# Performance work log

Hardware: AMD Instinct MI355X
Metric: run time of the kernel (lower is better)

Reference implementation:

```python
import jax, jax.numpy as jnp
import numpy as np
from jax import lax

NUM_HEADS = 4
DIM = 192
EPS = 1e-12  # torch F.normalize eps


def setup_inputs() -> dict:
    key = jax.random.key(0)
    ks = jax.random.split(key, 5)
    b, c, h, w = 8, DIM, 128, 128
    x = jax.random.normal(ks[0], (b, c, h, w), dtype=jnp.float32)
    f = jax.random.normal(ks[1], (b, c, h, w), dtype=jnp.float32)
    # conv weights, scaled like kaiming-ish init
    w_qkv = jax.random.normal(ks[2], (3 * c, c, 1, 1), dtype=jnp.float32) * (1.0 / np.sqrt(c))
    w_dw = jax.random.normal(ks[3], (3 * c, 1, 3, 3), dtype=jnp.float32) * (1.0 / 3.0)
    w_proj = jax.random.normal(ks[4], (c, c, 1, 1), dtype=jnp.float32) * (1.0 / np.sqrt(c))
    temperature = jnp.ones((NUM_HEADS, 1, 1), dtype=jnp.float32)
    return {"x": x, "f": f, "w_qkv": w_qkv, "w_dw": w_dw, "w_proj": w_proj,
            "temperature": temperature}


def _conv(x, w, groups=1):
    return lax.conv_general_dilated(
        x, w, window_strides=(1, 1), padding="SAME",
        dimension_numbers=("NCHW", "OIHW", "NCHW"),
        feature_group_count=groups)


def reference(x, f, w_qkv, w_dw, w_proj, temperature):
    b, c, h, w = x.shape
    x_in = x + f
    qkv = _conv(x_in, w_qkv)                 # [b, 3c, h, w] 1x1 conv
    qkv = _conv(qkv, w_dw, groups=3 * c)     # depthwise 3x3
    q, k, v = jnp.split(qkv, 3, axis=1)      # each [b, c, h, w]
    hw = h * w
    ch = c // NUM_HEADS

    def heads(t):
        return t.reshape(b, NUM_HEADS, ch, hw)  # 'b (head c) h w -> b head c (h w)'

    q, k, v = heads(q), heads(k), heads(v)
    # L2-normalize over spatial (last) dim, torch-style eps clamp
    q = q / jnp.maximum(jnp.linalg.norm(q, axis=-1, keepdims=True), EPS)
    k = k / jnp.maximum(jnp.linalg.norm(k, axis=-1, keepdims=True), EPS)
    # transposed (channel) attention: [b, head, ch, ch]
    attn = jnp.einsum("bhcn,bhdn->bhcd", q, k) * temperature[None]
    attn = jax.nn.softmax(attn, axis=-1)
    out = jnp.einsum("bhcd,bhdn->bhcn", attn, v)  # [b, head, ch, hw]
    out = out.reshape(b, c, h, w)
    return _conv(out, w_proj)
```

## Files before the change

### kernel.cpp

```cpp
#include <hip/hip_runtime.h>
#include <stdint.h>

#define NB 8
#define NC 192
#define NOC 576
#define NH 4
#define HW 16384
#define NCHUNK 16

typedef unsigned short u16;
typedef __bf16 v8bf __attribute__((ext_vector_type(8)));
typedef float v4f __attribute__((ext_vector_type(4)));
typedef u16 v8us __attribute__((ext_vector_type(8)));
typedef u16 v4us __attribute__((ext_vector_type(4)));

__device__ __forceinline__ u16 f2bf(float f) {
    uint32_t u = __float_as_uint(f);
    u += 0x7FFFu + ((u >> 16) & 1u);
    return (u16)(u >> 16);
}
__device__ __forceinline__ float bf2f(u16 u) {
    return __uint_as_float(((uint32_t)u) << 16);
}

__global__ void k_cvt_w(const float* __restrict__ w, u16* __restrict__ wb, int n) {
    int i = blockIdx.x * 256 + threadIdx.x;
    if (i < n) wb[i] = f2bf(w[i]);
}

__global__ __launch_bounds__(256, 2) void k_gemm_qkv(
    const float* __restrict__ x, const float* __restrict__ f,
    const u16* __restrict__ wb, u16* __restrict__ qkv, int b0)
{
    __shared__ u16 bt[64 * 192];
    __shared__ u16 wt[576 * 32];
    const int t = threadIdx.x;
    const int bl = blockIdx.y;
    const int bg = b0 + bl;
    const int p0 = blockIdx.x * 64;

    {
        const int px = t & 63;
        const int cg = t >> 6;
        #pragma unroll
        for (int it = 0; it < 6; ++it) {
            const int c4 = it * 4 + cg;
            const size_t base = ((size_t)bg * NC + c4 * 8) * HW + p0 + px;
            v8us pk;
            #pragma unroll
            for (int j = 0; j < 8; ++j) {
                float v = x[base + (size_t)j * HW] + f[base + (size_t)j * HW];
                pk[j] = f2bf(v);
            }
            *reinterpret_cast<v8us*>(&bt[px * 192 + ((c4 ^ (px & 7)) << 3)]) = pk;
        }
    }

    const int w = t >> 6, l = t & 63, lr = l & 15, lg = l >> 4;
    const int oc0 = w * 144;

    v4f acc[4][9];
    #pragma unroll
    for (int mi = 0; mi < 4; ++mi)
        #pragma unroll
        for (int ni = 0; ni < 9; ++ni)
            acc[mi][ni] = (v4f){0.f, 0.f, 0.f, 0.f};

    #pragma unroll 1
    for (int ks = 0; ks < 6; ++ks) {
        __syncthreads();
        #pragma unroll
        for (int it = 0; it < 9; ++it) {
            const int idx = it * 256 + t;
            const int oc = idx >> 2, lgw = idx & 3;
            v8us wv = *reinterpret_cast<const v8us*>(&wb[oc * 192 + ks * 32 + lgw * 8]);
            *reinterpret_cast<v8us*>(&wt[oc * 32 + ((lgw ^ ((oc >> 1) & 3)) << 3)]) = wv;
        }
        __syncthreads();

        v8bf a[4];
        #pragma unroll
        for (int mi = 0; mi < 4; ++mi) {
            const int px = mi * 16 + lr;
            a[mi] = *reinterpret_cast<const v8bf*>(&bt[px * 192 + (((ks * 4 + lg) ^ (px & 7)) << 3)]);
        }
        #pragma unroll
        for (int ni = 0; ni < 9; ++ni) {
            const int oc = oc0 + ni * 16 + lr;
            const v8bf bw = *reinterpret_cast<const v8bf*>(&wt[oc * 32 + ((lg ^ ((oc >> 1) & 3)) << 3)]);
            #pragma unroll
            for (int mi = 0; mi < 4; ++mi)
                acc[mi][ni] = __builtin_amdgcn_mfma_f32_16x16x32_bf16(a[mi], bw, acc[mi][ni], 0, 0, 0);
        }
    }

    #pragma unroll
    for (int mi = 0; mi < 4; ++mi)
        #pragma unroll
        for (int ni = 0; ni < 9; ++ni) {
            const int oc = oc0 + ni * 16 + lr;
            const int px = p0 + mi * 16 + lg * 4;
            v4us pk;
            pk[0] = f2bf(acc[mi][ni][0]); pk[1] = f2bf(acc[mi][ni][1]);
            pk[2] = f2bf(acc[mi][ni][2]); pk[3] = f2bf(acc[mi][ni][3]);
            *reinterpret_cast<v4us*>(&qkv[((size_t)bl * NOC + oc) * HW + px]) = pk;
        }
}

__global__ __launch_bounds__(256) void k_dw(
    const u16* __restrict__ qkv, const float* __restrict__ wdw,
    u16* __restrict__ qk_out, u16* __restrict__ v_out,
    float* __restrict__ sumsq, int b0)
{
    __shared__ u16 plane[128 * 136];
    __shared__ float red[4];
    const int t = threadIdx.x;
    const int ch = blockIdx.x;
    const int bl = blockIdx.y;
    const int bg = b0 + bl;
    const size_t pbase = ((size_t)bl * NOC + ch) * HW;

    float wk[9];
    #pragma unroll
    for (int i = 0; i < 9; ++i) wk[i] = wdw[ch * 9 + i];

    const int r = t >> 1;
    const int cb = (t & 1) * 64;

    #pragma unroll
    for (int i = 0; i < 8; ++i) {
        v8us v = *reinterpret_cast<const v8us*>(&qkv[pbase + r * 128 + cb + i * 8]);
        *reinterpret_cast<v8us*>(&plane[r * 136 + cb + i * 8]) = v;
    }
    __syncthreads();

    const bool vm = (r > 0), vp = (r < 127);
    const u16* rowm = &plane[(r - 1) * 136];
    const u16* rowc = &plane[r * 136];
    const u16* rowp = &plane[(r + 1) * 136];

    float am, ac, bm, bc, cm, cc2;
    if (cb == 0) { am = 0.f; bm = 0.f; cm = 0.f; }
    else {
        am = vm ? bf2f(rowm[cb - 1]) : 0.f;
        bm = bf2f(rowc[cb - 1]);
        cm = vp ? bf2f(rowp[cb - 1]) : 0.f;
    }
    ac = vm ? bf2f(rowm[cb]) : 0.f;
    bc = bf2f(rowc[cb]);
    cc2 = vp ? bf2f(rowp[cb]) : 0.f;

    uint32_t ov[32];
    float ssq = 0.f;
    #pragma unroll
    for (int xp = 0; xp < 32; ++xp) {
        #pragma unroll
        for (int s2 = 0; s2 < 2; ++s2) {
            const int col = cb + xp * 2 + s2;
            float ap, bp, cp;
            if (col < 127) {
                ap = vm ? bf2f(rowm[col + 1]) : 0.f;
                bp = bf2f(rowc[col + 1]);
                cp = vp ? bf2f(rowp[col + 1]) : 0.f;
            } else { ap = 0.f; bp = 0.f; cp = 0.f; }
            float o = wk[0]*am + wk[1]*ac + wk[2]*ap
                    + wk[3]*bm + wk[4]*bc + wk[5]*bp
                    + wk[6]*cm + wk[7]*cc2 + wk[8]*cp;
            u16 ob = f2bf(o);
            float orr = bf2f(ob);
            ssq += orr * orr;
            ov[xp] = (s2 == 0) ? (uint32_t)ob : (ov[xp] | ((uint32_t)ob << 16));
            am = ac; ac = ap; bm = bc; bc = bp; cm = cc2; cc2 = cp;
        }
    }

    __syncthreads();
    #pragma unroll
    for (int i = 0; i < 32; ++i)
        *reinterpret_cast<uint32_t*>(&plane[r * 136 + cb + i * 2]) = ov[i];
    __syncthreads();

    u16* dst = (ch < 2 * NC) ? (qk_out + ((size_t)bg * (2 * NC) + ch) * HW)
                             : (v_out + ((size_t)bg * NC + (ch - 2 * NC)) * HW);
    #pragma unroll
    for (int i = 0; i < 8; ++i) {
        const int idx = i * 2048 + t * 8;
        const int rr = idx >> 7, cc = idx & 127;
        v8us v = *reinterpret_cast<const v8us*>(&plane[rr * 136 + cc]);
        *reinterpret_cast<v8us*>(&dst[idx]) = v;
    }

    #pragma unroll
    for (int off = 32; off > 0; off >>= 1) ssq += __shfl_down(ssq, off);
    if ((t & 63) == 0) red[t >> 6] = ssq;
    __syncthreads();
    if (t == 0 && ch < 2 * NC) sumsq[bg * (2 * NC) + ch] = red[0] + red[1] + red[2] + red[3];
}

__global__ __launch_bounds__(256) void k_attn(
    const u16* __restrict__ qk, float* __restrict__ partials)
{
    __shared__ float wsum[4 * 2304];
    const int t = threadIdx.x;
    const int chunk = blockIdx.x;
    const int h = blockIdx.y;
    const int b = blockIdx.z;
    const int w = t >> 6, l = t & 63, lr = l & 15, lg = l >> 4;

    const size_t qbase = ((size_t)b * 384 + h * 48) * HW;
    const size_t kbase = ((size_t)b * 384 + 192 + h * 48) * HW;
    const int pb = chunk * 1024 + w * 256;

    v4f acc[3][3];
    #pragma unroll
    for (int mi = 0; mi < 3; ++mi)
        #pragma unroll
        for (int ni = 0; ni < 3; ++ni)
            acc[mi][ni] = (v4f){0.f, 0.f, 0.f, 0.f};

    #pragma unroll
    for (int ks = 0; ks < 8; ++ks) {
        const int k = pb + ks * 32 + lg * 8;
        v8bf a[3], bb[3];
        #pragma unroll
        for (int mi = 0; mi < 3; ++mi)
            a[mi] = *reinterpret_cast<const v8bf*>(&qk[qbase + (size_t)(mi * 16 + lr) * HW + k]);
        #pragma unroll
        for (int ni = 0; ni < 3; ++ni)
            bb[ni] = *reinterpret_cast<const v8bf*>(&qk[kbase + (size_t)(ni * 16 + lr) * HW + k]);
        #pragma unroll
        for (int mi = 0; mi < 3; ++mi)
            #pragma unroll
            for (int ni = 0; ni < 3; ++ni)
                acc[mi][ni] = __builtin_amdgcn_mfma_f32_16x16x32_bf16(a[mi], bb[ni], acc[mi][ni], 0, 0, 0);
    }

    #pragma unroll
    for (int mi = 0; mi < 3; ++mi)
        #pragma unroll
        for (int ni = 0; ni < 3; ++ni)
            #pragma unroll
            for (int r = 0; r < 4; ++r)
                wsum[w * 2304 + (mi * 16 + lg * 4 + r) * 48 + ni * 16 + lr] = acc[mi][ni][r];
    __syncthreads();

    #pragma unroll
    for (int i = 0; i < 9; ++i) {
        const int e = t + i * 256;
        float s = wsum[e] + wsum[2304 + e] + wsum[4608 + e] + wsum[6912 + e];
        partials[(((size_t)(b * NH + h)) * NCHUNK + chunk) * 2304 + e] = s;
    }
}

__global__ __launch_bounds__(256) void k_smx(
    const float* __restrict__ partials, const float* __restrict__ sumsq,
    const float* __restrict__ wproj, const float* __restrict__ temp,
    u16* __restrict__ Mb)
{
    __shared__ float att[2304];
    __shared__ float rq[48], rk[48];
    const int t = threadIdx.x;
    const int h = blockIdx.x;
    const int b = blockIdx.y;

    if (t < 48) {
        float s = sumsq[b * 384 + h * 48 + t];
        rq[t] = 1.f / fmaxf(sqrtf(s), 1e-12f);
    } else if (t < 96) {
        float s = sumsq[b * 384 + 192 + h * 48 + (t - 48)];
        rk[t - 48] = 1.f / fmaxf(sqrtf(s), 1e-12f);
    }
    __syncthreads();
    const float tp = temp[h];
    #pragma unroll
    for (int i = 0; i < 9; ++i) {
        const int e = t + i * 256;
        const float* pp = &partials[(((size_t)(b * NH + h)) * NCHUNK) * 2304 + e];
        float s = 0.f;
        #pragma unroll
        for (int c = 0; c < NCHUNK; ++c) s += pp[(size_t)c * 2304];
        att[e] = s * rq[e / 48] * rk[e % 48] * tp;
    }
    __syncthreads();
    if (t < 48) {
        float m = -1e30f;
        #pragma unroll
        for (int j = 0; j < 48; ++j) m = fmaxf(m, att[t * 48 + j]);
        float s = 0.f;
        for (int j = 0; j < 48; ++j) { float e2 = __expf(att[t * 48 + j] - m); att[t * 48 + j] = e2; s += e2; }
        const float inv = 1.f / s;
        for (int j = 0; j < 48; ++j) att[t * 48 + j] *= inv;
    }
    __syncthreads();
    #pragma unroll
    for (int i = 0; i < 36; ++i) {
        const int idx = t + i * 256;
        const int oc = idx / 48, d = idx % 48;
        float s = 0.f;
        #pragma unroll
        for (int cc = 0; cc < 48; ++cc)
            s += wproj[oc * 192 + h * 48 + cc] * att[cc * 48 + d];
        Mb[((size_t)b * NC + oc) * NC + h * 48 + d] = f2bf(s);
    }
}

__global__ __launch_bounds__(256) void k_gemm_out(
    const u16* __restrict__ vp, const u16* __restrict__ Mb,
    float* __restrict__ out)
{
    __shared__ u16 bt[64 * 192];
    const int t = threadIdx.x;
    const int b = blockIdx.y;
    const int p0 = blockIdx.x * 64;

    {
        const int px = t & 63;
        const int cg = t >> 6;
        #pragma unroll
        for (int it = 0; it < 6; ++it) {
            const int c4 = it * 4 + cg;
            const size_t base = ((size_t)b * NC + c4 * 8) * HW + p0 + px;
            v8us pk;
            #pragma unroll
            for (int j = 0; j < 8; ++j) pk[j] = vp[base + (size_t)j * HW];
            *reinterpret_cast<v8us*>(&bt[px * 192 + ((c4 ^ (px & 7)) << 3)]) = pk;
        }
    }
    __syncthreads();

    const int w = t >> 6, l = t & 63, lr = l & 15, lg = l >> 4;
    const int oc0 = w * 48;

    v4f acc[4][3];
    #pragma unroll
    for (int mi = 0; mi < 4; ++mi)
        #pragma unroll
        for (int ni = 0; ni < 3; ++ni)
            acc[mi][ni] = (v4f){0.f, 0.f, 0.f, 0.f};

    #pragma unroll
    for (int ks = 0; ks < 6; ++ks) {
        const int k = ks * 32 + lg * 8;
        const int c4 = ks * 4 + lg;
        v8bf a[4];
        #pragma unroll
        for (int mi = 0; mi < 4; ++mi) {
            const int px = mi * 16 + lr;
            a[mi] = *reinterpret_cast<const v8bf*>(&bt[px * 192 + ((c4 ^ (px & 7)) << 3)]);
        }
        #pragma unroll
        for (int ni = 0; ni < 3; ++ni) {
            const int oc = oc0 + ni * 16 + lr;
            const v8bf bw = *reinterpret_cast<const v8bf*>(&Mb[((size_t)b * NC + oc) * NC + k]);
            #pragma unroll
            for (int mi = 0; mi < 4; ++mi)
                acc[mi][ni] = __builtin_amdgcn_mfma_f32_16x16x32_bf16(a[mi], bw, acc[mi][ni], 0, 0, 0);
        }
    }

    #pragma unroll
    for (int mi = 0; mi < 4; ++mi)
        #pragma unroll
        for (int ni = 0; ni < 3; ++ni) {
            const int oc = oc0 + ni * 16 + lr;
            const int px = p0 + mi * 16 + lg * 4;
            *reinterpret_cast<v4f*>(&out[((size_t)b * NC + oc) * HW + px]) = acc[mi][ni];
        }
}

extern "C" void kernel_launch(void* const* d_in, const int* in_sizes, int n_in,
                              void* d_out, int out_size, void* d_ws, size_t ws_size,
                              hipStream_t stream)
{
    (void)in_sizes; (void)n_in; (void)out_size;
    const float* x      = (const float*)d_in[0];
    const float* f      = (const float*)d_in[1];
    const float* w_qkv  = (const float*)d_in[2];
    const float* w_dw   = (const float*)d_in[3];
    const float* w_proj = (const float*)d_in[4];
    const float* temp   = (const float*)d_in[5];

    char* ws = (char*)d_ws;
    u16*   vws      = (u16*)(ws);
    u16*   wb       = (u16*)(ws + 50331648);
    float* sumsq    = (float*)(ws + 50552832);
    float* partials = (float*)(ws + 50565120);
    u16*   Mb       = (u16*)(ws + 55283712);
    const size_t FIXED = 55873536;
    const size_t PERB  = (size_t)NOC * HW * 2;
    u16*   qkv_raw  = (u16*)(ws + FIXED);

    int g = 1;
    if (ws_size > FIXED + PERB) {
        size_t avail = (ws_size - FIXED) / PERB;
        g = (int)(avail > 8 ? 8 : avail);
        if (g < 1) g = 1;
    }

    u16* qk_scratch = (u16*)d_out;
    float* out      = (float*)d_out;

    hipLaunchKernelGGL(k_cvt_w, dim3(432), dim3(256), 0, stream, w_qkv, wb, NOC * NC);
    for (int b0 = 0; b0 < NB; b0 += g) {
        const int nb = (b0 + g <= NB) ? g : (NB - b0);
        hipLaunchKernelGGL(k_gemm_qkv, dim3(HW / 64, nb), dim3(256), 0, stream, x, f, wb, qkv_raw, b0);
        hipLaunchKernelGGL(k_dw, dim3(NOC, nb), dim3(256), 0, stream, qkv_raw, w_dw, qk_scratch, vws, sumsq, b0);
    }
    hipLaunchKernelGGL(k_attn, dim3(NCHUNK, NH, NB), dim3(256), 0, stream, qk_scratch, partials);
    hipLaunchKernelGGL(k_smx, dim3(NH, NB), dim3(256), 0, stream, partials, sumsq, w_proj, temp, Mb);
    hipLaunchKernelGGL(k_gemm_out, dim3(HW / 64, NB), dim3(256), 0, stream, vws, Mb, out);
}
```

Before: 333.5 us.

## Prefetch next weight slice into registers and stage qkv stores through LDS

The 1x1 conv kernel now loads the next K-slice of weights into registers while the current slice is consumed, which hides global load latency behind MFMA work. The epilogue writes accumulators into the LDS weight buffer with an XOR swizzle, then reads them back so each thread emits contiguous 16-byte global stores instead of scattered 8-byte ones. This costs 36 extra VGPRs for the prefetch buffer and two extra barrier pairs in the epilogue. The higher register pressure may lower occupancy.

```diff
diff --git a/kernel.cpp b/kernel.cpp
--- a/kernel.cpp
+++ b/kernel.cpp
@@ -66,6 +66,16 @@
         for (int ni = 0; ni < 9; ++ni)
             acc[mi][ni] = (v4f){0.f, 0.f, 0.f, 0.f};
 
+    const int widx_oc = (t * 4) >> 2;
+
+    v8us wload[9];
+    #pragma unroll
+    for (int it = 0; it < 9; ++it) {
+        const int idx = it * 256 + t;
+        const int oc = idx >> 2, lgw = idx & 3;
+        wload[it] = *reinterpret_cast<const v8us*>(&wb[oc * 192 + lgw * 8]);
+    }
+
     #pragma unroll 1
     for (int ks = 0; ks < 6; ++ks) {
         __syncthreads();
@@ -73,8 +83,15 @@
         for (int it = 0; it < 9; ++it) {
             const int idx = it * 256 + t;
             const int oc = idx >> 2, lgw = idx & 3;
-            v8us wv = *reinterpret_cast<const v8us*>(&wb[oc * 192 + ks * 32 + lgw * 8]);
-            *reinterpret_cast<v8us*>(&wt[oc * 32 + ((lgw ^ ((oc >> 1) & 3)) << 3)]) = wv;
+            *reinterpret_cast<v8us*>(&wt[oc * 32 + ((lgw ^ ((oc >> 1) & 3)) << 3)]) = wload[it];
+        }
+        if (ks < 5) {
+            #pragma unroll
+            for (int it = 0; it < 9; ++it) {
+                const int idx = it * 256 + t;
+                const int oc = idx >> 2, lgw = idx & 3;
+                wload[it] = *reinterpret_cast<const v8us*>(&wb[oc * 192 + (ks + 1) * 32 + lgw * 8]);
+            }
         }
         __syncthreads();
 
@@ -95,16 +112,39 @@
     }
 
     #pragma unroll
-    for (int mi = 0; mi < 4; ++mi)
-        #pragma unroll
-        for (int ni = 0; ni < 9; ++ni) {
-            const int oc = oc0 + ni * 16 + lr;
-            const int px = p0 + mi * 16 + lg * 4;
-            v4us pk;
-            pk[0] = f2bf(acc[mi][ni][0]); pk[1] = f2bf(acc[mi][ni][1]);
-            pk[2] = f2bf(acc[mi][ni][2]); pk[3] = f2bf(acc[mi][ni][3]);
-            *reinterpret_cast<v4us*>(&qkv[((size_t)bl * NOC + oc) * HW + px]) = pk;
-        }
+    for (int pass = 0; pass < 2; ++pass) {
+        __syncthreads();
+        #pragma unroll
+        for (int mi2 = 0; mi2 < 2; ++mi2) {
+            const int mi = pass * 2 + mi2;
+            #pragma unroll
+            for (int ni = 0; ni < 9; ++ni) {
+                const int oc = oc0 + ni * 16 + lr;
+                const int chunk = mi2 * 4 + lg;
+                const int sch = chunk ^ (oc & 3);
+                v4us pk;
+                pk[0] = f2bf(acc[mi][ni][0]); pk[1] = f2bf(acc[mi][ni][1]);
+                pk[2] = f2bf(acc[mi][ni][2]); pk[3] = f2bf(acc[mi][ni][3]);
+                *reinterpret_cast<v4us*>(&wt[oc * 32 + sch * 4]) = pk;
+            }
+        }
+        __syncthreads();
+        #pragma unroll
+        for (int rd = 0; rd < 9; ++rd) {
+            const int e = rd * 2048 + t * 8;
+            const int oc = e >> 5;
+            const int col = e & 31;
+            const int c0 = (col >> 2) ^ (oc & 3);
+            const int c1 = ((col >> 2) + 1) ^ (oc & 3);
+            v4us lo = *reinterpret_cast<v4us*>(&wt[oc * 32 + c0 * 4]);
+            v4us hi = *reinterpret_cast<v4us*>(&wt[oc * 32 + c1 * 4]);
+            v8us o8;
+            o8[0] = lo[0]; o8[1] = lo[1]; o8[2] = lo[2]; o8[3] = lo[3];
+            o8[4] = hi[0]; o8[5] = hi[1]; o8[6] = hi[2]; o8[7] = hi[3];
+            *reinterpret_cast<v8us*>(&qkv[((size_t)bl * NOC + oc) * HW + p0 + pass * 32 + col]) = o8;
+        }
+    }
+    (void)widx_oc;
 }
 
 __global__ __launch_bounds__(256) void k_dw(
```

Result: faster. 310.0 us (-7.1%).

## Use 512-thread QKV GEMM blocks with prefetched weights and LDS-staged output stores

Applied to the files above, without the earlier changes.

The QKV 1x1-conv GEMM kernel moves from 256 to 512 threads per block, splitting the 64-pixel tile across two wave groups so each wave keeps half as many accumulators. Weight K-slices are prefetched into registers one step ahead so global loads overlap the MFMA work, and the LDS swizzle for weights changes. The output is staged through shared memory so each channel row is written as contiguous 64-byte segments instead of scattered 8-byte pieces. This adds extra barriers and LDS traffic in the epilogue, and occupancy at 4 blocks per CU may be limited by the roughly 48KB of LDS each block uses.

```diff
diff --git a/kernel.cpp b/kernel.cpp
--- a/kernel.cpp
+++ b/kernel.cpp
@@ -28,7 +28,7 @@
     if (i < n) wb[i] = f2bf(w[i]);
 }
 
-__global__ __launch_bounds__(256, 2) void k_gemm_qkv(
+__global__ __launch_bounds__(512, 4) void k_gemm_qkv(
     const float* __restrict__ x, const float* __restrict__ f,
     const u16* __restrict__ wb, u16* __restrict__ qkv, int b0)
 {
@@ -43,8 +43,8 @@
         const int px = t & 63;
         const int cg = t >> 6;
         #pragma unroll
-        for (int it = 0; it < 6; ++it) {
-            const int c4 = it * 4 + cg;
+        for (int it = 0; it < 3; ++it) {
+            const int c4 = it * 8 + cg;
             const size_t base = ((size_t)bg * NC + c4 * 8) * HW + p0 + px;
             v8us pk;
             #pragma unroll
@@ -57,54 +57,96 @@
     }
 
     const int w = t >> 6, l = t & 63, lr = l & 15, lg = l >> 4;
-    const int oc0 = w * 144;
-
-    v4f acc[4][9];
-    #pragma unroll
-    for (int mi = 0; mi < 4; ++mi)
+    const int wp = w >> 2;
+    const int wo = w & 3;
+    const int oc0 = wo * 144;
+
+    v4f acc[2][9];
+    #pragma unroll
+    for (int mi = 0; mi < 2; ++mi)
         #pragma unroll
         for (int ni = 0; ni < 9; ++ni)
             acc[mi][ni] = (v4f){0.f, 0.f, 0.f, 0.f};
+
+    v8us wload[5];
+    #pragma unroll
+    for (int it = 0; it < 5; ++it) {
+        const int idx = it * 512 + t;
+        if (idx < 2304) {
+            const int oc = idx >> 2, q = idx & 3;
+            wload[it] = *reinterpret_cast<const v8us*>(&wb[oc * 192 + q * 8]);
+        }
+    }
 
     #pragma unroll 1
     for (int ks = 0; ks < 6; ++ks) {
         __syncthreads();
         #pragma unroll
-        for (int it = 0; it < 9; ++it) {
-            const int idx = it * 256 + t;
-            const int oc = idx >> 2, lgw = idx & 3;
-            v8us wv = *reinterpret_cast<const v8us*>(&wb[oc * 192 + ks * 32 + lgw * 8]);
-            *reinterpret_cast<v8us*>(&wt[oc * 32 + ((lgw ^ ((oc >> 1) & 3)) << 3)]) = wv;
+        for (int it = 0; it < 5; ++it) {
+            const int idx = it * 512 + t;
+            if (idx < 2304) {
+                const int oc = idx >> 2, q = idx & 3;
+                const int g = (oc ^ (oc >> 2)) & 3;
+                *reinterpret_cast<v8us*>(&wt[oc * 32 + ((q ^ g) << 3)]) = wload[it];
+            }
+        }
+        if (ks < 5) {
+            #pragma unroll
+            for (int it = 0; it < 5; ++it) {
+                const int idx = it * 512 + t;
+                if (idx < 2304) {
+                    const int oc = idx >> 2, q = idx & 3;
+                    wload[it] = *reinterpret_cast<const v8us*>(&wb[oc * 192 + (ks + 1) * 32 + q * 8]);
+                }
+            }
         }
         __syncthreads();
 
-        v8bf a[4];
-        #pragma unroll
-        for (int mi = 0; mi < 4; ++mi) {
-            const int px = mi * 16 + lr;
+        v8bf a[2];
+        #pragma unroll
+        for (int mi = 0; mi < 2; ++mi) {
+            const int px = wp * 32 + mi * 16 + lr;
             a[mi] = *reinterpret_cast<const v8bf*>(&bt[px * 192 + (((ks * 4 + lg) ^ (px & 7)) << 3)]);
         }
         #pragma unroll
         for (int ni = 0; ni < 9; ++ni) {
             const int oc = oc0 + ni * 16 + lr;
-            const v8bf bw = *reinterpret_cast<const v8bf*>(&wt[oc * 32 + ((lg ^ ((oc >> 1) & 3)) << 3)]);
-            #pragma unroll
-            for (int mi = 0; mi < 4; ++mi)
+            const int g = (oc ^ (oc >> 2)) & 3;
+            const v8bf bw = *reinterpret_cast<const v8bf*>(&wt[oc * 32 + ((lg ^ g) << 3)]);
+            #pragma unroll
+            for (int mi = 0; mi < 2; ++mi)
                 acc[mi][ni] = __builtin_amdgcn_mfma_f32_16x16x32_bf16(a[mi], bw, acc[mi][ni], 0, 0, 0);
         }
     }
 
     #pragma unroll
-    for (int mi = 0; mi < 4; ++mi)
-        #pragma unroll
-        for (int ni = 0; ni < 9; ++ni) {
-            const int oc = oc0 + ni * 16 + lr;
-            const int px = p0 + mi * 16 + lg * 4;
-            v4us pk;
-            pk[0] = f2bf(acc[mi][ni][0]); pk[1] = f2bf(acc[mi][ni][1]);
-            pk[2] = f2bf(acc[mi][ni][2]); pk[3] = f2bf(acc[mi][ni][3]);
-            *reinterpret_cast<v4us*>(&qkv[((size_t)bl * NOC + oc) * HW + px]) = pk;
-        }
+    for (int pass = 0; pass < 2; ++pass) {
+        __syncthreads();
+        if (wp == pass) {
+            #pragma unroll
+            for (int mi = 0; mi < 2; ++mi) {
+                #pragma unroll
+                for (int ni = 0; ni < 9; ++ni) {
+                    const int oc = oc0 + ni * 16 + lr;
+                    const int chunk = mi * 4 + lg;
+                    const int sch = chunk ^ (oc & 7);
+                    v4us pk;
+                    pk[0] = f2bf(acc[mi][ni][0]); pk[1] = f2bf(acc[mi][ni][1]);
+                    pk[2] = f2bf(acc[mi][ni][2]); pk[3] = f2bf(acc[mi][ni][3]);
+                    *reinterpret_cast<v4us*>(&wt[oc * 32 + sch * 4]) = pk;
+                }
+            }
+        }
+        __syncthreads();
+        #pragma unroll
+        for (int rd = 0; rd < 9; ++rd) {
+            const int idx = rd * 512 + t;
+            const int oc = idx >> 3;
+            const int c = idx & 7;
+            v4us v = *reinterpret_cast<v4us*>(&wt[oc * 32 + (c ^ (oc & 7)) * 4]);
+            *reinterpret_cast<v4us*>(&qkv[((size_t)bl * NOC + oc) * HW + p0 + pass * 32 + c * 4]) = v;
+        }
+    }
 }
 
 __global__ __launch_bounds__(256) void k_dw(
@@ -403,7 +445,7 @@
     hipLaunchKernelGGL(k_cvt_w, dim3(432), dim3(256), 0, stream, w_qkv, wb, NOC * NC);
     for (int b0 = 0; b0 < NB; b0 += g) {
         const int nb = (b0 + g <= NB) ? g : (NB - b0);
-        hipLaunchKernelGGL(k_gemm_qkv, dim3(HW / 64, nb), dim3(256), 0, stream, x, f, wb, qkv_raw, b0);
+        hipLaunchKernelGGL(k_gemm_qkv, dim3(HW / 64, nb), dim3(512), 0, stream, x, f, wb, qkv_raw, b0);
         hipLaunchKernelGGL(k_dw, dim3(NOC, nb), dim3(256), 0, stream, qkv_raw, w_dw, qk_scratch, vws, sumsq, b0);
     }
     hipLaunchKernelGGL(k_attn, dim3(NCHUNK, NH, NB), dim3(256), 0, stream, qk_scratch, partials);
```

Result: faster. 301.7 us (-9.5%).

## Fuse QKV 1x1 GEMM with depthwise 3x3 via row-ring shared buffer

Applied to the files above, without the earlier changes.

Replaces the separate QKV GEMM and depthwise-conv kernels with a prep kernel that writes x+f as channel-last bf16, plus a fused kernel. The fused kernel computes 1x1-conv rows into a 4-slot shared-memory ring and immediately applies the 3x3 depthwise stencil. It writes outputs in a row-group-blocked layout with per-group partial sums of squares, which the softmax kernel then reduces. This removes the round trip of the full 576-channel intermediate through global memory, at the cost of recomputing halo rows (10 rows per 8) and reading weights directly from global. The output GEMM now stages its results through LDS to make the stores coalesced.

```diff
diff --git a/kernel.cpp b/kernel.cpp
--- a/kernel.cpp
+++ b/kernel.cpp
@@ -7,6 +7,10 @@
 #define NH 4
 #define HW 16384
 #define NCHUNK 16
+#define NRG 16
+#define RPG 8
+#define NOCG 6
+#define OCG 96
 
 typedef unsigned short u16;
 typedef __bf16 v8bf __attribute__((ext_vector_type(8)));
@@ -28,173 +32,164 @@
     if (i < n) wb[i] = f2bf(w[i]);
 }
 
-__global__ __launch_bounds__(256, 2) void k_gemm_qkv(
+__global__ __launch_bounds__(256) void k_prep(
     const float* __restrict__ x, const float* __restrict__ f,
-    const u16* __restrict__ wb, u16* __restrict__ qkv, int b0)
-{
-    __shared__ u16 bt[64 * 192];
-    __shared__ u16 wt[576 * 32];
+    u16* __restrict__ xf)
+{
+    __shared__ u16 xt[128 * 200];
     const int t = threadIdx.x;
-    const int bl = blockIdx.y;
-    const int bg = b0 + bl;
-    const int p0 = blockIdx.x * 64;
-
-    {
-        const int px = t & 63;
-        const int cg = t >> 6;
-        #pragma unroll
-        for (int it = 0; it < 6; ++it) {
-            const int c4 = it * 4 + cg;
-            const size_t base = ((size_t)bg * NC + c4 * 8) * HW + p0 + px;
-            v8us pk;
-            #pragma unroll
-            for (int j = 0; j < 8; ++j) {
-                float v = x[base + (size_t)j * HW] + f[base + (size_t)j * HW];
-                pk[j] = f2bf(v);
+    const int row = blockIdx.x;
+    const int bg = blockIdx.y;
+
+    #pragma unroll
+    for (int it = 0; it < 24; ++it) {
+        const int idx = it * 256 + t;
+        const int q = idx & 31;
+        const int c = idx >> 5;
+        const size_t base = ((size_t)bg * NC + c) * HW + row * 128 + q * 4;
+        const float4 xv = *reinterpret_cast<const float4*>(&x[base]);
+        const float4 fv = *reinterpret_cast<const float4*>(&f[base]);
+        xt[(q * 4 + 0) * 200 + c] = f2bf(xv.x + fv.x);
+        xt[(q * 4 + 1) * 200 + c] = f2bf(xv.y + fv.y);
+        xt[(q * 4 + 2) * 200 + c] = f2bf(xv.z + fv.z);
+        xt[(q * 4 + 3) * 200 + c] = f2bf(xv.w + fv.w);
+    }
+    __syncthreads();
+    if (t < 192) {
+        const int co = t % 24;
+        const int pxg = t / 24;
+        #pragma unroll
+        for (int it = 0; it < 16; ++it) {
+            const int px = it * 8 + pxg;
+            v8us v = *reinterpret_cast<v8us*>(&xt[px * 200 + co * 8]);
+            *reinterpret_cast<v8us*>(&xf[((size_t)(bg * 128 + row) * 128 + px) * 192 + co * 8]) = v;
+        }
+    }
+}
+
+__global__ __launch_bounds__(512) void k_fused(
+    const u16* __restrict__ xf, const u16* __restrict__ wb,
+    const float* __restrict__ wdw,
+    u16* __restrict__ qk_t, u16* __restrict__ v_t,
+    float* __restrict__ sumsqp)
+{
+    __shared__ u16 ring[4 * 96 * 136];
+    const int t = threadIdx.x;
+    const int ocg = blockIdx.x / NRG;
+    const int rg  = blockIdx.x % NRG;
+    const int bg  = blockIdx.y;
+    const int r0 = rg * RPG;
+    const int oc_base = ocg * OCG;
+
+    const int w = t >> 6, l = t & 63, lr = l & 15, lg = l >> 4;
+    const int wpx = w & 3;
+    const int woc = w >> 1 & 0;
+    const int wo2 = w >> 2;
+
+    const int oc_l = t >> 2;
+    const int px0 = (t & 3) * 32;
+    float wk[9];
+    if (t < 384) {
+        #pragma unroll
+        for (int i = 0; i < 9; ++i) wk[i] = wdw[(oc_base + oc_l) * 9 + i];
+    }
+    float ssq = 0.f;
+
+    #pragma unroll 1
+    for (int rr = r0 - 1; rr <= r0 + RPG; ++rr) {
+        if (rr >= 0 && rr < 128) {
+            v4f acc[2][3];
+            #pragma unroll
+            for (int mi = 0; mi < 2; ++mi)
+                #pragma unroll
+                for (int ni = 0; ni < 3; ++ni)
+                    acc[mi][ni] = (v4f){0.f, 0.f, 0.f, 0.f};
+            #pragma unroll
+            for (int ks = 0; ks < 6; ++ks) {
+                v8bf a[2];
+                #pragma unroll
+                for (int mi = 0; mi < 2; ++mi)
+                    a[mi] = *reinterpret_cast<const v8bf*>(
+                        &xf[((size_t)(bg * 128 + rr) * 128 + wpx * 32 + mi * 16 + lr) * 192 + ks * 32 + lg * 8]);
+                #pragma unroll
+                for (int ni = 0; ni < 3; ++ni) {
+                    const v8bf bw = *reinterpret_cast<const v8bf*>(
+                        &wb[(size_t)(oc_base + wo2 * 48 + ni * 16 + lr) * 192 + ks * 32 + lg * 8]);
+                    #pragma unroll
+                    for (int mi = 0; mi < 2; ++mi)
+                        acc[mi][ni] = __builtin_amdgcn_mfma_f32_16x16x32_bf16(a[mi], bw, acc[mi][ni], 0, 0, 0);
+                }
             }
-            *reinterpret_cast<v8us*>(&bt[px * 192 + ((c4 ^ (px & 7)) << 3)]) = pk;
-        }
-    }
-
-    const int w = t >> 6, l = t & 63, lr = l & 15, lg = l >> 4;
-    const int oc0 = w * 144;
-
-    v4f acc[4][9];
-    #pragma unroll
-    for (int mi = 0; mi < 4; ++mi)
-        #pragma unroll
-        for (int ni = 0; ni < 9; ++ni)
-            acc[mi][ni] = (v4f){0.f, 0.f, 0.f, 0.f};
-
-    #pragma unroll 1
-    for (int ks = 0; ks < 6; ++ks) {
+            const int slot = (rr & 3) * (96 * 136);
+            #pragma unroll
+            for (int mi = 0; mi < 2; ++mi)
+                #pragma unroll
+                for (int ni = 0; ni < 3; ++ni) {
+                    const int ol = wo2 * 48 + ni * 16 + lr;
+                    const int pxw = wpx * 32 + mi * 16 + lg * 4;
+                    v4us pk;
+                    pk[0] = f2bf(acc[mi][ni][0]); pk[1] = f2bf(acc[mi][ni][1]);
+                    pk[2] = f2bf(acc[mi][ni][2]); pk[3] = f2bf(acc[mi][ni][3]);
+                    *reinterpret_cast<v4us*>(&ring[slot + ol * 136 + pxw]) = pk;
+                }
+        }
         __syncthreads();
-        #pragma unroll
-        for (int it = 0; it < 9; ++it) {
-            const int idx = it * 256 + t;
-            const int oc = idx >> 2, lgw = idx & 3;
-            v8us wv = *reinterpret_cast<const v8us*>(&wb[oc * 192 + ks * 32 + lgw * 8]);
-            *reinterpret_cast<v8us*>(&wt[oc * 32 + ((lgw ^ ((oc >> 1) & 3)) << 3)]) = wv;
-        }
-        __syncthreads();
-
-        v8bf a[4];
-        #pragma unroll
-        for (int mi = 0; mi < 4; ++mi) {
-            const int px = mi * 16 + lr;
-            a[mi] = *reinterpret_cast<const v8bf*>(&bt[px * 192 + (((ks * 4 + lg) ^ (px & 7)) << 3)]);
-        }
-        #pragma unroll
-        for (int ni = 0; ni < 9; ++ni) {
-            const int oc = oc0 + ni * 16 + lr;
-            const v8bf bw = *reinterpret_cast<const v8bf*>(&wt[oc * 32 + ((lg ^ ((oc >> 1) & 3)) << 3)]);
-            #pragma unroll
-            for (int mi = 0; mi < 4; ++mi)
-                acc[mi][ni] = __builtin_amdgcn_mfma_f32_16x16x32_bf16(a[mi], bw, acc[mi][ni], 0, 0, 0);
-        }
-    }
-
-    #pragma unroll
-    for (int mi = 0; mi < 4; ++mi)
-        #pragma unroll
-        for (int ni = 0; ni < 9; ++ni) {
-            const int oc = oc0 + ni * 16 + lr;
-            const int px = p0 + mi * 16 + lg * 4;
-            v4us pk;
-            pk[0] = f2bf(acc[mi][ni][0]); pk[1] = f2bf(acc[mi][ni][1]);
-            pk[2] = f2bf(acc[mi][ni][2]); pk[3] = f2bf(acc[mi][ni][3]);
-            *reinterpret_cast<v4us*>(&qkv[((size_t)bl * NOC + oc) * HW + px]) = pk;
-        }
-}
-
-__global__ __launch_bounds__(256) void k_dw(
-    const u16* __restrict__ qkv, const float* __restrict__ wdw,
-    u16* __restrict__ qk_out, u16* __restrict__ v_out,
-    float* __restrict__ sumsq, int b0)
-{
-    __shared__ u16 plane[128 * 136];
-    __shared__ float red[4];
-    const int t = threadIdx.x;
-    const int ch = blockIdx.x;
-    const int bl = blockIdx.y;
-    const int bg = b0 + bl;
-    const size_t pbase = ((size_t)bl * NOC + ch) * HW;
-
-    float wk[9];
-    #pragma unroll
-    for (int i = 0; i < 9; ++i) wk[i] = wdw[ch * 9 + i];
-
-    const int r = t >> 1;
-    const int cb = (t & 1) * 64;
-
-    #pragma unroll
-    for (int i = 0; i < 8; ++i) {
-        v8us v = *reinterpret_cast<const v8us*>(&qkv[pbase + r * 128 + cb + i * 8]);
-        *reinterpret_cast<v8us*>(&plane[r * 136 + cb + i * 8]) = v;
-    }
-    __syncthreads();
-
-    const bool vm = (r > 0), vp = (r < 127);
-    const u16* rowm = &plane[(r - 1) * 136];
-    const u16* rowc = &plane[r * 136];
-    const u16* rowp = &plane[(r + 1) * 136];
-
-    float am, ac, bm, bc, cm, cc2;
-    if (cb == 0) { am = 0.f; bm = 0.f; cm = 0.f; }
-    else {
-        am = vm ? bf2f(rowm[cb - 1]) : 0.f;
-        bm = bf2f(rowc[cb - 1]);
-        cm = vp ? bf2f(rowp[cb - 1]) : 0.f;
-    }
-    ac = vm ? bf2f(rowm[cb]) : 0.f;
-    bc = bf2f(rowc[cb]);
-    cc2 = vp ? bf2f(rowp[cb]) : 0.f;
-
-    uint32_t ov[32];
-    float ssq = 0.f;
-    #pragma unroll
-    for (int xp = 0; xp < 32; ++xp) {
-        #pragma unroll
-        for (int s2 = 0; s2 < 2; ++s2) {
-            const int col = cb + xp * 2 + s2;
-            float ap, bp, cp;
-            if (col < 127) {
-                ap = vm ? bf2f(rowm[col + 1]) : 0.f;
-                bp = bf2f(rowc[col + 1]);
-                cp = vp ? bf2f(rowp[col + 1]) : 0.f;
-            } else { ap = 0.f; bp = 0.f; cp = 0.f; }
-            float o = wk[0]*am + wk[1]*ac + wk[2]*ap
-                    + wk[3]*bm + wk[4]*bc + wk[5]*bp
-                    + wk[6]*cm + wk[7]*cc2 + wk[8]*cp;
-            u16 ob = f2bf(o);
-            float orr = bf2f(ob);
-            ssq += orr * orr;
-            ov[xp] = (s2 == 0) ? (uint32_t)ob : (ov[xp] | ((uint32_t)ob << 16));
-            am = ac; ac = ap; bm = bc; bc = bp; cm = cc2; cc2 = cp;
-        }
-    }
-
-    __syncthreads();
-    #pragma unroll
-    for (int i = 0; i < 32; ++i)
-        *reinterpret_cast<uint32_t*>(&plane[r * 136 + cb + i * 2]) = ov[i];
-    __syncthreads();
-
-    u16* dst = (ch < 2 * NC) ? (qk_out + ((size_t)bg * (2 * NC) + ch) * HW)
-                             : (v_out + ((size_t)bg * NC + (ch - 2 * NC)) * HW);
-    #pragma unroll
-    for (int i = 0; i < 8; ++i) {
-        const int idx = i * 2048 + t * 8;
-        const int rr = idx >> 7, cc = idx & 127;
-        v8us v = *reinterpret_cast<const v8us*>(&plane[rr * 136 + cc]);
-        *reinterpret_cast<v8us*>(&dst[idx]) = v;
-    }
-
-    #pragma unroll
-    for (int off = 32; off > 0; off >>= 1) ssq += __shfl_down(ssq, off);
-    if ((t & 63) == 0) red[t >> 6] = ssq;
-    __syncthreads();
-    if (t == 0 && ch < 2 * NC) sumsq[bg * (2 * NC) + ch] = red[0] + red[1] + red[2] + red[3];
+        const int rd = rr - 1;
+        if (rd >= r0 && rd < r0 + RPG && t < 384) {
+            const u16* rowm = &ring[((rd - 1) & 3) * (96 * 136) + oc_l * 136];
+            const u16* rowc = &ring[((rd    ) & 3) * (96 * 136) + oc_l * 136];
+            const u16* rowp = &ring[((rd + 1) & 3) * (96 * 136) + oc_l * 136];
+            const bool vm = (rd > 0), vp = (rd < 127);
+
+            float am, ac, bm, bc, cm, cc2;
+            if (px0 == 0) { am = 0.f; bm = 0.f; cm = 0.f; }
+            else {
+                am = vm ? bf2f(rowm[px0 - 1]) : 0.f;
+                bm = bf2f(rowc[px0 - 1]);
+                cm = vp ? bf2f(rowp[px0 - 1]) : 0.f;
+            }
+            ac = vm ? bf2f(rowm[px0]) : 0.f;
+            bc = bf2f(rowc[px0]);
+            cc2 = vp ? bf2f(rowp[px0]) : 0.f;
+
+            uint32_t ov[16];
+            #pragma unroll
+            for (int xp = 0; xp < 16; ++xp) {
+                #pragma unroll
+                for (int s2 = 0; s2 < 2; ++s2) {
+                    const int col = px0 + xp * 2 + s2;
+                    float ap, bp, cp;
+                    if (col < 127) {
+                        ap = vm ? bf2f(rowm[col + 1]) : 0.f;
+                        bp = bf2f(rowc[col + 1]);
+                        cp = vp ? bf2f(rowp[col + 1]) : 0.f;
+                    } else { ap = 0.f; bp = 0.f; cp = 0.f; }
+                    float o = wk[0]*am + wk[1]*ac + wk[2]*ap
+                            + wk[3]*bm + wk[4]*bc + wk[5]*bp
+                            + wk[6]*cm + wk[7]*cc2 + wk[8]*cp;
+                    u16 ob = f2bf(o);
+                    float orr = bf2f(ob);
+                    ssq += orr * orr;
+                    ov[xp] = (s2 == 0) ? (uint32_t)ob : (ov[xp] | ((uint32_t)ob << 16));
+                    am = ac; ac = ap; bm = bc; bc = bp; cm = cc2; cc2 = cp;
+                }
+            }
+
+            u16* dst = (ocg < 4)
+                ? qk_t + ((size_t)(bg * NRG + rg) * 384 + ocg * 96 + oc_l) * 1024 + (rd & 7) * 128 + px0
+                : v_t  + ((size_t)(bg * NRG + rg) * 192 + (ocg - 4) * 96 + oc_l) * 1024 + (rd & 7) * 128 + px0;
+            #pragma unroll
+            for (int k2 = 0; k2 < 4; ++k2)
+                *reinterpret_cast<uint4*>(dst + k2 * 8) = *reinterpret_cast<uint4*>(&ov[k2 * 4]);
+        }
+    }
+
+    if (ocg < 4 && t < 384) {
+        ssq += __shfl_down(ssq, 2);
+        ssq += __shfl_down(ssq, 1);
+        if ((t & 3) == 0)
+            sumsqp[((size_t)rg * NB + bg) * 384 + ocg * 96 + oc_l] = ssq;
+    }
 }
 
 __global__ __launch_bounds__(256) void k_attn(
@@ -207,9 +202,9 @@
     const int b = blockIdx.z;
     const int w = t >> 6, l = t & 63, lr = l & 15, lg = l >> 4;
 
-    const size_t qbase = ((size_t)b * 384 + h * 48) * HW;
-    const size_t kbase = ((size_t)b * 384 + 192 + h * 48) * HW;
-    const int pb = chunk * 1024 + w * 256;
+    const size_t qbase = ((size_t)(b * NRG + chunk) * 384 + h * 48) * 1024;
+    const size_t kbase = ((size_t)(b * NRG + chunk) * 384 + 192 + h * 48) * 1024;
+    const int pb = w * 256;
 
     v4f acc[3][3];
     #pragma unroll
@@ -224,10 +219,10 @@
         v8bf a[3], bb[3];
         #pragma unroll
         for (int mi = 0; mi < 3; ++mi)
-            a[mi] = *reinterpret_cast<const v8bf*>(&qk[qbase + (size_t)(mi * 16 + lr) * HW + k]);
+            a[mi] = *reinterpret_cast<const v8bf*>(&qk[qbase + (size_t)(mi * 16 + lr) * 1024 + k]);
         #pragma unroll
         for (int ni = 0; ni < 3; ++ni)
-            bb[ni] = *reinterpret_cast<const v8bf*>(&qk[kbase + (size_t)(ni * 16 + lr) * HW + k]);
+            bb[ni] = *reinterpret_cast<const v8bf*>(&qk[kbase + (size_t)(ni * 16 + lr) * 1024 + k]);
         #pragma unroll
         for (int mi = 0; mi < 3; ++mi)
             #pragma unroll
@@ -253,7 +248,7 @@
 }
 
 __global__ __launch_bounds__(256) void k_smx(
-    const float* __restrict__ partials, const float* __restrict__ sumsq,
+    const float* __restrict__ partials, const float* __restrict__ sumsqp,
     const float* __restrict__ wproj, const float* __restrict__ temp,
     u16* __restrict__ Mb)
 {
@@ -264,10 +259,16 @@
     const int b = blockIdx.y;
 
     if (t < 48) {
-        float s = sumsq[b * 384 + h * 48 + t];
+        float s = 0.f;
+        #pragma unroll
+        for (int rg = 0; rg < NRG; ++rg)
+            s += sumsqp[((size_t)rg * NB + b) * 384 + h * 48 + t];
         rq[t] = 1.f / fmaxf(sqrtf(s), 1e-12f);
     } else if (t < 96) {
-        float s = sumsq[b * 384 + 192 + h * 48 + (t - 48)];
+        float s = 0.f;
+        #pragma unroll
+        for (int rg = 0; rg < NRG; ++rg)
+            s += sumsqp[((size_t)rg * NB + b) * 384 + 192 + h * 48 + (t - 48)];
         rk[t - 48] = 1.f / fmaxf(sqrtf(s), 1e-12f);
     }
     __syncthreads();
@@ -308,10 +309,12 @@
     const u16* __restrict__ vp, const u16* __restrict__ Mb,
     float* __restrict__ out)
 {
-    __shared__ u16 bt[64 * 192];
+    __shared__ float smemf[12288];
+    u16* bt = reinterpret_cast<u16*>(smemf);
     const int t = threadIdx.x;
     const int b = blockIdx.y;
     const int p0 = blockIdx.x * 64;
+    const int row = p0 >> 7, rgo = row >> 3, rl = row & 7, c0 = p0 & 127;
 
     {
         const int px = t & 63;
@@ -319,10 +322,10 @@
         #pragma unroll
         for (int it = 0; it < 6; ++it) {
             const int c4 = it * 4 + cg;
-            const size_t base = ((size_t)b * NC + c4 * 8) * HW + p0 + px;
             v8us pk;
             #pragma unroll
-            for (int j = 0; j < 8; ++j) pk[j] = vp[base + (size_t)j * HW];
+            for (int j = 0; j < 8; ++j)
+                pk[j] = vp[((size_t)(b * NRG + rgo) * 192 + c4 * 8 + j) * 1024 + rl * 128 + c0 + px];
             *reinterpret_cast<v8us*>(&bt[px * 192 + ((c4 ^ (px & 7)) << 3)]) = pk;
         }
     }
@@ -358,21 +361,34 @@
         }
     }
 
+    __syncthreads();
+    float* et = smemf;
     #pragma unroll
     for (int mi = 0; mi < 4; ++mi)
         #pragma unroll
         for (int ni = 0; ni < 3; ++ni) {
             const int oc = oc0 + ni * 16 + lr;
-            const int px = p0 + mi * 16 + lg * 4;
-            *reinterpret_cast<v4f*>(&out[((size_t)b * NC + oc) * HW + px]) = acc[mi][ni];
-        }
+            const int u = mi * 4 + lg;
+            const int su = u ^ (oc & 15);
+            *reinterpret_cast<v4f*>(&et[oc * 64 + su * 4]) = acc[mi][ni];
+        }
+    __syncthreads();
+    #pragma unroll
+    for (int rd = 0; rd < 12; ++rd) {
+        const int idx = rd * 256 + t;
+        const int oc = idx >> 4;
+        const int u = idx & 15;
+        const int su = u ^ (oc & 15);
+        v4f v = *reinterpret_cast<v4f*>(&et[oc * 64 + su * 4]);
+        *reinterpret_cast<v4f*>(&out[((size_t)b * NC + oc) * HW + p0 + u * 4]) = v;
+    }
 }
 
 extern "C" void kernel_launch(void* const* d_in, const int* in_sizes, int n_in,
                               void* d_out, int out_size, void* d_ws, size_t ws_size,
                               hipStream_t stream)
 {
-    (void)in_sizes; (void)n_in; (void)out_size;
+    (void)in_sizes; (void)n_in; (void)out_size; (void)ws_size;
     const float* x      = (const float*)d_in[0];
     const float* f      = (const float*)d_in[1];
     const float* w_qkv  = (const float*)d_in[2];
@@ -383,30 +399,19 @@
     char* ws = (char*)d_ws;
     u16*   vws      = (u16*)(ws);
     u16*   wb       = (u16*)(ws + 50331648);
-    float* sumsq    = (float*)(ws + 50552832);
-    float* partials = (float*)(ws + 50565120);
-    u16*   Mb       = (u16*)(ws + 55283712);
-    const size_t FIXED = 55873536;
-    const size_t PERB  = (size_t)NOC * HW * 2;
-    u16*   qkv_raw  = (u16*)(ws + FIXED);
-
-    int g = 1;
-    if (ws_size > FIXED + PERB) {
-        size_t avail = (ws_size - FIXED) / PERB;
-        g = (int)(avail > 8 ? 8 : avail);
-        if (g < 1) g = 1;
-    }
-
-    u16* qk_scratch = (u16*)d_out;
-    float* out      = (float*)d_out;
+    float* sumsqp   = (float*)(ws + 50552832);
+    float* partials = (float*)(ws + 50749440);
+    u16*   Mb       = (u16*)(ws + 55468032);
+    u16*   xf       = (u16*)(ws + 56057856);
+
+    u16* qk_t = (u16*)d_out;
+    float* out = (float*)d_out;
 
     hipLaunchKernelGGL(k_cvt_w, dim3(432), dim3(256), 0, stream, w_qkv, wb, NOC * NC);
-    for (int b0 = 0; b0 < NB; b0 += g) {
-        const int nb = (b0 + g <= NB) ? g : (NB - b0);
-        hipLaunchKernelGGL(k_gemm_qkv, dim3(HW / 64, nb), dim3(256), 0, stream, x, f, wb, qkv_raw, b0);
-        hipLaunchKernelGGL(k_dw, dim3(NOC, nb), dim3(256), 0, stream, qkv_raw, w_dw, qk_scratch, vws, sumsq, b0);
-    }
-    hipLaunchKernelGGL(k_attn, dim3(NCHUNK, NH, NB), dim3(256), 0, stream, qk_scratch, partials);
-    hipLaunchKernelGGL(k_smx, dim3(NH, NB), dim3(256), 0, stream, partials, sumsq, w_proj, temp, Mb);
+    hipLaunchKernelGGL(k_prep, dim3(128, NB), dim3(256), 0, stream, x, f, xf);
+    hipLaunchKernelGGL(k_fused, dim3(NOCG * NRG, NB), dim3(512), 0, stream,
+                       xf, wb, w_dw, qk_t, vws, sumsqp);
+    hipLaunchKernelGGL(k_attn, dim3(NCHUNK, NH, NB), dim3(256), 0, stream, qk_t, partials);
+    hipLaunchKernelGGL(k_smx, dim3(NH, NB), dim3(256), 0, stream, partials, sumsqp, w_proj, temp, Mb);
     hipLaunchKernelGGL(k_gemm_out, dim3(HW / 64, NB), dim3(256), 0, stream, vws, Mb, out);
 }
```

Measured after the change: 430.6 us. 1.29x slower.
